# Kernel optimization log

Measured on AMD Instinct MI355X. Metric: run time of the kernel, lower is better.

The kernel has to match this reference:

```python
import jax, jax.numpy as jnp
import numpy as np

N = 100_000      # nodes
E = 1_600_000    # edges (avg degree 16)
IN = 128
H = 128
OUT = 2
G = 512          # graphs in the batch


def setup_inputs() -> dict:
    key = jax.random.key(0)
    ks = jax.random.split(key, 10)
    x = jax.random.normal(ks[0], (N, IN), dtype=jnp.float32)
    edge_index = jax.random.randint(ks[1], (2, E), 0, N, dtype=jnp.int64)
    edge_weight = jax.random.uniform(ks[2], (E,), dtype=jnp.float32)
    batch = jnp.sort(jax.random.randint(ks[3], (N,), 0, G, dtype=jnp.int64))
    s_in = 1.0 / np.sqrt(IN)
    s_h = 1.0 / np.sqrt(H)
    W1 = jax.random.normal(ks[4], (IN, H), dtype=jnp.float32) * s_in
    b1 = jnp.zeros((H,), dtype=jnp.float32)
    W2 = jax.random.normal(ks[5], (H, H), dtype=jnp.float32) * s_h
    b2 = jnp.zeros((H,), dtype=jnp.float32)
    Wl = jax.random.normal(ks[6], (H, OUT), dtype=jnp.float32) * s_h
    bl = jnp.zeros((OUT,), dtype=jnp.float32)
    return {"x": x, "edge_index": edge_index, "edge_weight": edge_weight,
            "batch": batch, "W1": W1, "b1": b1, "W2": W2, "b2": b2,
            "Wl": Wl, "bl": bl}


def _gcn_layer(x, W, b, row, col, ew, n):
    # PyG GCNConv: linear transform, symmetric-normalized scatter-add, bias.
    xw = x @ W                                           # [n, H]
    deg = jax.ops.segment_sum(ew, col, num_segments=n)    # weighted in-degree
    dis = jnp.where(deg > 0, jax.lax.rsqrt(deg), 0.0)
    norm = dis[row] * ew * dis[col]                       # [E+n]
    msg = xw[row] * norm[:, None]                         # gather + scale
    out = jax.ops.segment_sum(msg, col, num_segments=n)   # scatter-add to targets
    return out + b


def reference(x, edge_index, edge_weight, batch, W1, b1, W2, b2, Wl, bl):
    n = x.shape[0]
    # GCNConv default: add self-loops with weight 1.0 (gcn_norm fill_value=1)
    loop = jnp.arange(n, dtype=edge_index.dtype)
    row = jnp.concatenate([edge_index[0], loop])
    col = jnp.concatenate([edge_index[1], loop])
    ew = jnp.concatenate([edge_weight, jnp.ones((n,), edge_weight.dtype)])

    h = jax.nn.relu(_gcn_layer(x, W1, b1, row, col, ew, n))
    h = jax.nn.relu(_gcn_layer(h, W2, b2, row, col, ew, n))

    # global_mean_pool over batch ids
    cnt = jax.ops.segment_sum(jnp.ones((n,), h.dtype), batch, num_segments=G)
    pooled = jax.ops.segment_sum(h, batch, num_segments=G)
    pooled = pooled / jnp.maximum(cnt, 1.0)[:, None]      # [G, H]

    return pooled @ Wl + bl                               # [G, OUT]
```

## Files before the change

### kernel.cpp

```cpp
#include <hip/hip_runtime.h>
#include <hip/hip_fp16.h>


#define HDIM 128
typedef unsigned int uint;
typedef unsigned long long u64;
typedef _Float16 half8 __attribute__((ext_vector_type(8)));
typedef float f32x4 __attribute__((ext_vector_type(4)));
typedef float f32x2 __attribute__((ext_vector_type(2)));

#define NBUCK 391
#define BSTRIDE 8192
#define SCAT_BLOCKS 392
#define CHUNK 4096
#define QITER 16

template <typename AT>
__device__ __forceinline__ void gemm_body(
    const AT* __restrict__ A, const float* __restrict__ W,
    unsigned char* __restrict__ Y, int n, int nstrip, int tid, int bid,
    int nblk, char* smem) {
  char* Wt = smem;
  for (int t = tid; t < 2048; t += 256) {
    int c = t & 127;
    int k8 = t >> 7;
    const float* wp = W + (size_t)(k8 * 8) * HDIM + c;
    half8 hv;
#pragma unroll
    for (int m = 0; m < 8; ++m) hv[m] = (_Float16)wp[m * HDIM];
    int byte = c * 256 + k8 * 16;
    byte ^= ((c & 7) << 4);
    *(half8*)&Wt[byte] = hv;
  }
  __syncthreads();

  int wave = tid >> 6, lane = tid & 63;
  int l15 = lane & 15, l4 = lane >> 4;
  char* ep = smem + 32768 + wave * 2048;
  int stride = nblk * 4;
  for (int s = bid * 4 + wave; s < nstrip; s += stride) {
    int row0 = s << 4;
    int xrl = min(row0 + l15, n - 1);
    half8 bf[4];
    if constexpr (sizeof(AT) == 4) {
      const float* ap = (const float*)A + (size_t)xrl * HDIM + l4 * 8;
#pragma unroll
      for (int kk = 0; kk < 4; ++kk) {
        float4 u = *(const float4*)(ap + kk * 32);
        float4 v = *(const float4*)(ap + kk * 32 + 4);
        half8 h;
        h[0] = (_Float16)u.x; h[1] = (_Float16)u.y;
        h[2] = (_Float16)u.z; h[3] = (_Float16)u.w;
        h[4] = (_Float16)v.x; h[5] = (_Float16)v.y;
        h[6] = (_Float16)v.z; h[7] = (_Float16)v.w;
        bf[kk] = h;
      }
    } else {
      const half8* ap = (const half8*)((const _Float16*)A + (size_t)xrl * HDIM + l4 * 8);
#pragma unroll
      for (int kk = 0; kk < 4; ++kk) bf[kk] = ap[kk * 4];
    }
    f32x4 acc[8];
#pragma unroll
    for (int cf = 0; cf < 8; ++cf) acc[cf] = (f32x4){0.f, 0.f, 0.f, 0.f};
#pragma unroll
    for (int kk = 0; kk < 4; ++kk) {
#pragma unroll
      for (int cf = 0; cf < 8; ++cf) {
        int c = cf * 16 + l15;
        int byte = c * 256 + kk * 64 + l4 * 16;
        byte ^= ((c & 7) << 4);
        half8 af = *(half8*)&Wt[byte];
        acc[cf] = __builtin_amdgcn_mfma_f32_16x16x32_f16(af, bf[kk], acc[cf], 0, 0, 0);
      }
    }
#pragma unroll
    for (int cf = 0; cf < 8; ++cf) {
      int w = 0;
      w = __builtin_amdgcn_cvt_pk_fp8_f32(acc[cf][0], acc[cf][1], w, false);
      w = __builtin_amdgcn_cvt_pk_fp8_f32(acc[cf][2], acc[cf][3], w, true);
      int byte = l15 * 128 + ((cf * 16) ^ ((l15 & 7) << 4)) + l4 * 4;
      *(int*)&ep[byte] = w;
    }
    asm volatile("s_waitcnt lgkmcnt(0)" ::: "memory");
#pragma unroll
    for (int p = 0; p < 2; ++p) {
      int rl = p * 8 + (lane >> 3);
      int c16 = (lane & 7) * 16;
      int byte = rl * 128 + (c16 ^ ((rl & 7) << 4));
      uint4 v = *(uint4*)&ep[byte];
      int orow = row0 + rl;
      if (orow < n)
        *(uint4*)(Y + (size_t)orow * 128 + c16) = v;
    }
    asm volatile("s_waitcnt lgkmcnt(0)" ::: "memory");
  }
}

__global__ __launch_bounds__(256) void init_gstart_kernel(
    uint* __restrict__ gcur, const int* __restrict__ batch,
    int* __restrict__ start, int n, int G) {
  int bid = blockIdx.x, tid = threadIdx.x;
  if (bid < 2) {
    int t = bid * 256 + tid;
    if (t < NBUCK) gcur[t] = (uint)(t * BSTRIDE);
    return;
  }
  int i = (bid - 2) * 256 + tid;
  if (i >= n) return;
  int b = batch[i];
  if (i == 0) {
    for (int h = 0; h <= b; ++h) start[h] = 0;
  } else {
    int bp = batch[i - 1];
    for (int h = bp + 1; h <= b; ++h) start[h] = i;
  }
  if (i == n - 1) {
    for (int h = b + 1; h <= G; ++h) start[h] = n;
  }
}

__global__ __launch_bounds__(256) void scatter_gemm1_kernel(
    const int* __restrict__ row, const int* __restrict__ col,
    const float* __restrict__ ew, uint* __restrict__ gcur,
    uint2* __restrict__ rec, int E,
    const float* __restrict__ A, const float* __restrict__ W,
    unsigned char* __restrict__ Y, int n, int nstrip, int GBLK) {
  __shared__ __align__(16) char smem[40960];
  int bid = blockIdx.x, tid = threadIdx.x;
  if (bid % 3 == 0) {
    int sidx = bid / 3;
    uint* cntL = (uint*)smem;
    uint* baseL = cntL + NBUCK;
    for (int t = tid; t < NBUCK; t += 256) cntL[t] = 0;
    __syncthreads();
    int e0 = sidx * CHUNK + tid;
    uint pk[QITER];
#pragma unroll
    for (int q = 0; q < QITER; ++q) {
      int e = e0 + q * 256;
      pk[q] = 0xFFFFFFFFu;
      if (e < E) {
        uint c = (uint)col[e];
        uint b = c >> 8;
        uint r = atomicAdd(&cntL[b], 1u);
        pk[q] = (b << 21) | ((c & 255u) << 13) | r;
      }
    }
    __syncthreads();
    for (int t = tid; t < NBUCK; t += 256) {
      uint c = cntL[t];
      baseL[t] = c ? atomicAdd(&gcur[t], c) : 0;
    }
    __syncthreads();
#pragma unroll
    for (int q = 0; q < QITER; ++q) {
      int e = e0 + q * 256;
      if (e < E) {
        uint b = pk[q] >> 21;
        uint clo = (pk[q] >> 13) & 255u;
        uint rk = pk[q] & 8191u;
        uint slot = baseL[b] + rk;
        rec[slot] = make_uint2(((uint)row[e] << 8) | clo,
                               __float_as_uint(ew[e]));
      }
    }
    return;
  }
  int gidx = bid - bid / 3 - 1;
  gemm_body<float>(A, W, Y, n, nstrip, tid, gidx, GBLK, smem);
}

__global__ __launch_bounds__(512) void scan_buckets_kernel(
    const uint* __restrict__ gcur, uint* __restrict__ cbase,
    int* __restrict__ off, int n, int E) {
  __shared__ uint tmp[512];
  int tid = threadIdx.x;
  uint v = (tid < NBUCK) ? (gcur[tid] - (uint)(tid * BSTRIDE)) : 0;
  tmp[tid] = v;
  __syncthreads();
  for (int d = 1; d < 512; d <<= 1) {
    uint t = (tid >= d) ? tmp[tid - d] : 0;
    __syncthreads();
    tmp[tid] += t;
    __syncthreads();
  }
  if (tid < NBUCK) cbase[tid] = tmp[tid] - v;
  if (tid == 0) off[n] = E;
}

__global__ __launch_bounds__(256) void bucket_stats_kernel(
    const uint2* __restrict__ rec, const uint* __restrict__ gcur,
    const uint* __restrict__ cbase, float* __restrict__ dis,
    int* __restrict__ off, int n) {
  __shared__ uint degL[256];
  __shared__ uint cntL[256];
  __shared__ uint scn[256];
  int b = blockIdx.x, tid = threadIdx.x;
  degL[tid] = 0;
  cntL[tid] = 0;
  __syncthreads();
  uint s = (uint)(b * BSTRIDE);
  uint e = gcur[b];
  for (uint i = s + tid; i < e; i += 256) {
    uint2 r = rec[i];
    uint cl = r.x & 255u;
    atomicAdd(&cntL[cl], 1u);
    atomicAdd(&degL[cl], __float2uint_rn(__uint_as_float(r.y) * 65536.0f));
  }
  __syncthreads();
  uint v = cntL[tid];
  scn[tid] = v;
  __syncthreads();
  for (int d = 1; d < 256; d <<= 1) {
    uint t = (tid >= d) ? scn[tid - d] : 0;
    __syncthreads();
    scn[tid] += t;
    __syncthreads();
  }
  int c = b * 256 + tid;
  if (c < n) {
    off[c] = (int)(cbase[b] + scn[tid] - v);
    float deg = (float)degL[tid] * (1.0f / 65536.0f);
    dis[c] = rsqrtf(deg + 1.0f);
  }
}

__global__ __launch_bounds__(256) void csr_fill_kernel(
    const uint2* __restrict__ rec, const uint* __restrict__ gcur,
    const float* __restrict__ dis, const int* __restrict__ off,
    uint* __restrict__ csr, int n) {
  __shared__ uint baseL[256];
  __shared__ uint curL[256];
  int b = blockIdx.x, tid = threadIdx.x;
  int c = b * 256 + tid;
  baseL[tid] = (c < n) ? (uint)off[c] : 0;
  curL[tid] = 0;
  __syncthreads();
  uint s = (uint)(b * BSTRIDE);
  uint e = gcur[b];
  for (uint i = s + tid; i < e; i += 256) {
    uint2 rcd = rec[i];
    uint cl = rcd.x & 255u;
    uint r = rcd.x >> 8;
    uint slot = baseL[cl] + atomicAdd(&curL[cl], 1u);
    float ewv = __uint_as_float(rcd.y);
    uint nq = __float2uint_rn(dis[r] * ewv * 32768.0f);
    nq = min(nq, 32767u);
    csr[slot] = (r << 15) | nq;
  }
}

__global__ __launch_bounds__(256) void gemm_mfma_kernel(
    const _Float16* __restrict__ A, const float* __restrict__ W,
    unsigned char* __restrict__ Y, int n, int nstrip) {
  __shared__ __align__(16) char smem[40960];
  gemm_body<_Float16>(A, W, Y, n, nstrip, threadIdx.x, blockIdx.x, gridDim.x, smem);
}

__global__ __launch_bounds__(256) void agg_kernel(
    const uint* __restrict__ xw, const uint* __restrict__ csr,
    const float* __restrict__ dis, const int* __restrict__ off,
    const float* __restrict__ bias, uint* __restrict__ out, int n) {
  int node = blockIdx.x * 4 + (threadIdx.x >> 6);
  if (node >= n) return;
  int lane = threadIdx.x & 63;
  int hl = lane & 31;
  int par = lane >> 5;
  float dc = dis[node];
  float a0, a1, a2, a3;
  {
    uint v = xw[(size_t)node * 32 + hl];
    f32x2 lo = __builtin_amdgcn_cvt_pk_f32_fp8((int)v, false);
    f32x2 hi = __builtin_amdgcn_cvt_pk_f32_fp8((int)v, true);
    float sd = (par == 0) ? dc : 0.0f;
    a0 = sd * lo[0]; a1 = sd * lo[1]; a2 = sd * hi[0]; a3 = sd * hi[1];
  }
  const float qs = 1.0f / 32768.0f;
  int s = off[node], t = off[node + 1];
  int i = s;
  for (; i + 16 <= t; i += 16) {
    uint ee[8];
#pragma unroll
    for (int j = 0; j < 8; ++j) ee[j] = csr[i + 2 * j + par];
    uint vv[8];
#pragma unroll
    for (int j = 0; j < 8; ++j) vv[j] = xw[(size_t)(ee[j] >> 15) * 32 + hl];
#pragma unroll
    for (int j = 0; j < 8; ++j) {
      float nn = (float)(ee[j] & 0x7FFFu) * qs;
      f32x2 lo = __builtin_amdgcn_cvt_pk_f32_fp8((int)vv[j], false);
      f32x2 hi = __builtin_amdgcn_cvt_pk_f32_fp8((int)vv[j], true);
      a0 += nn * lo[0]; a1 += nn * lo[1]; a2 += nn * hi[0]; a3 += nn * hi[1];
    }
  }
  for (; i + 8 <= t; i += 8) {
    uint ee[4];
#pragma unroll
    for (int j = 0; j < 4; ++j) ee[j] = csr[i + 2 * j + par];
    uint vv[4];
#pragma unroll
    for (int j = 0; j < 4; ++j) vv[j] = xw[(size_t)(ee[j] >> 15) * 32 + hl];
#pragma unroll
    for (int j = 0; j < 4; ++j) {
      float nn = (float)(ee[j] & 0x7FFFu) * qs;
      f32x2 lo = __builtin_amdgcn_cvt_pk_f32_fp8((int)vv[j], false);
      f32x2 hi = __builtin_amdgcn_cvt_pk_f32_fp8((int)vv[j], true);
      a0 += nn * lo[0]; a1 += nn * lo[1]; a2 += nn * hi[0]; a3 += nn * hi[1];
    }
  }
  for (; i < t; i += 2) {
    if (i + par < t) {
      uint e = csr[i + par];
      uint v = xw[(size_t)(e >> 15) * 32 + hl];
      float nn = (float)(e & 0x7FFFu) * qs;
      f32x2 lo = __builtin_amdgcn_cvt_pk_f32_fp8((int)v, false);
      f32x2 hi = __builtin_amdgcn_cvt_pk_f32_fp8((int)v, true);
      a0 += nn * lo[0]; a1 += nn * lo[1]; a2 += nn * hi[0]; a3 += nn * hi[1];
    }
  }
  a0 += __shfl_xor(a0, 32);
  a1 += __shfl_xor(a1, 32);
  a2 += __shfl_xor(a2, 32);
  a3 += __shfl_xor(a3, 32);
  if (par == 0) {
    float4 b = *(const float4*)(bias + hl * 4);
    a0 = fmaxf(dc * a0 + b.x, 0.0f);
    a1 = fmaxf(dc * a1 + b.y, 0.0f);
    a2 = fmaxf(dc * a2 + b.z, 0.0f);
    a3 = fmaxf(dc * a3 + b.w, 0.0f);
    __half2 p0 = __floats2half2_rn(a0, a1);
    __half2 p1 = __floats2half2_rn(a2, a3);
    ((uint2*)out)[(size_t)node * 32 + hl] = make_uint2(*(uint*)&p0, *(uint*)&p1);
  }
}

__global__ __launch_bounds__(256) void pool_final_kernel(
    const uint* __restrict__ h, const int* __restrict__ start,
    const float* __restrict__ Wl, const float* __restrict__ bl,
    float* __restrict__ out) {
  __shared__ float2 red[256];
  int g = blockIdx.x;
  int grp = threadIdx.x >> 6, f = threadIdx.x & 63;
  int s = start[g], e = start[g + 1];
  float s0 = 0.0f, s1 = 0.0f;
  for (int r = s + grp; r < e; r += 4) {
    uint v = h[((size_t)r << 6) + f];
    float2 fv = __half22float2(*(const __half2*)&v);
    s0 += fv.x;
    s1 += fv.y;
  }
  red[threadIdx.x] = make_float2(s0, s1);
  __syncthreads();
  if (grp == 0) {
    float2 a = red[f], b = red[64 + f], c = red[128 + f], d = red[192 + f];
    float inv = 1.0f / (float)max(e - s, 1);
    float pv0 = (a.x + b.x + c.x + d.x) * inv;
    float pv1 = (a.y + b.y + c.y + d.y) * inv;
#pragma unroll
    for (int o = 0; o < 2; ++o) {
      float sdot = pv0 * Wl[4 * f + o] + pv1 * Wl[4 * f + 2 + o];
      for (int d2 = 32; d2 > 0; d2 >>= 1) sdot += __shfl_down(sdot, d2);
      if (f == 0) out[g * 2 + o] = sdot + bl[o];
    }
  }
}

extern "C" void kernel_launch(void* const* d_in, const int* in_sizes, int n_in,
                              void* d_out, int out_size, void* d_ws, size_t ws_size,
                              hipStream_t stream) {
  const float* x     = (const float*)d_in[0];
  const int*   ei    = (const int*)d_in[1];
  const float* ew    = (const float*)d_in[2];
  const int*   batch = (const int*)d_in[3];
  const float* W1    = (const float*)d_in[4];
  const float* b1    = (const float*)d_in[5];
  const float* W2    = (const float*)d_in[6];
  const float* b2    = (const float*)d_in[7];
  const float* Wl    = (const float*)d_in[8];
  const float* bl    = (const float*)d_in[9];
  float* out = (float*)d_out;

  const int N = in_sizes[0] / HDIM;
  const int E = in_sizes[2];
  const int G = out_size / 2;

  const int* row = ei;
  const int* col = ei + E;

  auto al = [](size_t v) { return (v + 255) & ~(size_t)255; };
  char* ws = (char*)d_ws;
  size_t o_gcur   = 0;
  size_t o_cbase  = o_gcur   + al(NBUCK * 4);
  size_t o_start  = o_cbase  + al(NBUCK * 4);
  size_t o_off    = o_start  + al(((size_t)G + 1) * 4);
  size_t o_dis    = o_off    + al(((size_t)N + 1) * 4);
  size_t o_rec    = o_dis    + al((size_t)N * 4);
  size_t o_csr    = o_rec    + al((size_t)NBUCK * BSTRIDE * 8);
  size_t o_xw     = o_csr    + al((size_t)E * 4);
  size_t o_h      = o_xw     + al((size_t)N * 128);

  uint*  gcur    = (uint*) (ws + o_gcur);
  uint*  cbase   = (uint*) (ws + o_cbase);
  int*   start   = (int*)  (ws + o_start);
  int*   off     = (int*)  (ws + o_off);
  float* dis     = (float*)(ws + o_dis);
  uint2* rec     = (uint2*)(ws + o_rec);
  uint*  csr     = (uint*) (ws + o_csr);
  unsigned char* xw = (unsigned char*)(ws + o_xw);
  uint*  hbuf    = (uint*) (ws + o_h);

  int NBg = (N + 255) / 256;
  int nstrip = (N + 15) / 16;
  int MB  = 1024;
  int AB  = (N + 3) / 4;
  int TOTAL_C = SCAT_BLOCKS * 3;
  int GBLK = TOTAL_C - SCAT_BLOCKS;

  init_gstart_kernel<<<2 + NBg, 256, 0, stream>>>(gcur, batch, start, N, G);

  scatter_gemm1_kernel<<<TOTAL_C, 256, 0, stream>>>(
      row, col, ew, gcur, rec, E, x, W1, xw, N, nstrip, GBLK);

  scan_buckets_kernel<<<1, 512, 0, stream>>>(gcur, cbase, off, N, E);

  bucket_stats_kernel<<<NBUCK, 256, 0, stream>>>(rec, gcur, cbase, dis, off, N);

  csr_fill_kernel<<<NBUCK, 256, 0, stream>>>(rec, gcur, dis, off, csr, N);

  agg_kernel<<<AB, 256, 0, stream>>>((const uint*)xw, csr, dis, off, b1, hbuf, N);

  gemm_mfma_kernel<<<MB, 256, 0, stream>>>((const _Float16*)hbuf, W2, xw, N, nstrip);
  agg_kernel<<<AB, 256, 0, stream>>>((const uint*)xw, csr, dis, off, b2, hbuf, N);

  pool_final_kernel<<<G, 256, 0, stream>>>(hbuf, start, Wl, bl, out);
}
```

Baseline: 201.6 us.

## Fold source normalization into xw rows, merge stats/fill, coalesce bucket scatter

Scatter blocks now stage their records in shared memory sorted by bucket and write them out contiguously, so global writes coalesce instead of landing at random slots. The bucket-stats and CSR-fill kernels are merged into one kernel. That kernel also pre-scales the layer-1 xw rows by the source node's dis, so the CSR weight no longer needs a random dis[row] gather. The layer-2 GEMM applies the same dis scaling in its epilogue. This saves a launch and scattered reads, at the cost of an extra read-modify-write pass over xw and fp8 re-quantisation after scaling, which may lose accuracy.

```diff
diff --git a/kernel.cpp b/kernel.cpp
--- a/kernel.cpp
+++ b/kernel.cpp
@@ -15,11 +15,11 @@
 #define CHUNK 4096
 #define QITER 16
 
-template <typename AT>
+template <typename AT, bool SCALE>
 __device__ __forceinline__ void gemm_body(
     const AT* __restrict__ A, const float* __restrict__ W,
-    unsigned char* __restrict__ Y, int n, int nstrip, int tid, int bid,
-    int nblk, char* smem) {
+    unsigned char* __restrict__ Y, const float* __restrict__ dsc,
+    int n, int nstrip, int tid, int bid, int nblk, char* smem) {
   char* Wt = smem;
   for (int t = tid; t < 2048; t += 256) {
     int c = t & 127;
@@ -74,11 +74,13 @@
         acc[cf] = __builtin_amdgcn_mfma_f32_16x16x32_f16(af, bf[kk], acc[cf], 0, 0, 0);
       }
     }
+    float ds = 1.0f;
+    if constexpr (SCALE) ds = dsc[xrl];
 #pragma unroll
     for (int cf = 0; cf < 8; ++cf) {
       int w = 0;
-      w = __builtin_amdgcn_cvt_pk_fp8_f32(acc[cf][0], acc[cf][1], w, false);
-      w = __builtin_amdgcn_cvt_pk_fp8_f32(acc[cf][2], acc[cf][3], w, true);
+      w = __builtin_amdgcn_cvt_pk_fp8_f32(acc[cf][0] * ds, acc[cf][1] * ds, w, false);
+      w = __builtin_amdgcn_cvt_pk_fp8_f32(acc[cf][2] * ds, acc[cf][3] * ds, w, true);
       int byte = l15 * 128 + ((cf * 16) ^ ((l15 & 7) << 4)) + l4 * 4;
       *(int*)&ep[byte] = w;
     }
@@ -130,8 +132,11 @@
   int bid = blockIdx.x, tid = threadIdx.x;
   if (bid % 3 == 0) {
     int sidx = bid / 3;
-    uint* cntL = (uint*)smem;
-    uint* baseL = cntL + NBUCK;
+    uint* cntL  = (uint*)smem;
+    uint* sbase = (uint*)(smem + 1568);
+    uint* gdel  = (uint*)(smem + 3136);
+    uint2* recL = (uint2*)(smem + 4736);
+    uint* tmp   = (uint*)(smem + 4736);
     for (int t = tid; t < NBUCK; t += 256) cntL[t] = 0;
     __syncthreads();
     int e0 = sidx * CHUNK + tid;
@@ -148,9 +153,28 @@
       }
     }
     __syncthreads();
+    uint v0 = (tid < NBUCK) ? cntL[tid] : 0;
+    uint v1 = (tid + 256 < NBUCK) ? cntL[tid + 256] : 0;
+    tmp[tid] = v0;
+    tmp[tid + 256] = v1;
+    __syncthreads();
+    for (int d = 1; d < 512; d <<= 1) {
+      uint a0 = (tid >= d) ? tmp[tid - d] : 0;
+      uint a1 = (tid + 256 >= d) ? tmp[tid + 256 - d] : 0;
+      __syncthreads();
+      tmp[tid] += a0;
+      tmp[tid + 256] += a1;
+      __syncthreads();
+    }
+    if (tid < NBUCK) sbase[tid] = tmp[tid] - v0;
+    if (tid + 256 < NBUCK) sbase[tid + 256] = tmp[tid + 256] - v1;
+    if (tid == NBUCK - 1 - 256) sbase[NBUCK] = tmp[NBUCK - 1];
+    __syncthreads();
+    uint tcount = sbase[NBUCK];
     for (int t = tid; t < NBUCK; t += 256) {
       uint c = cntL[t];
-      baseL[t] = c ? atomicAdd(&gcur[t], c) : 0;
+      uint gb = c ? atomicAdd(&gcur[t], c) : 0;
+      gdel[t] = gb - sbase[t];
     }
     __syncthreads();
 #pragma unroll
@@ -160,15 +184,27 @@
         uint b = pk[q] >> 21;
         uint clo = (pk[q] >> 13) & 255u;
         uint rk = pk[q] & 8191u;
-        uint slot = baseL[b] + rk;
-        rec[slot] = make_uint2(((uint)row[e] << 8) | clo,
-                               __float_as_uint(ew[e]));
+        recL[sbase[b] + rk] = make_uint2(((uint)row[e] << 8) | clo,
+                                         __float_as_uint(ew[e]));
       }
     }
+    __syncthreads();
+#pragma unroll
+    for (int q = 0; q < QITER; ++q) {
+      uint p = (uint)(q * 256 + tid);
+      if (p < tcount) {
+        int lo = 0, hi = NBUCK;
+        while (hi - lo > 1) {
+          int mid = (lo + hi) >> 1;
+          if (p >= sbase[mid]) lo = mid; else hi = mid;
+        }
+        rec[p + gdel[lo]] = recL[p];
+      }
+    }
     return;
   }
   int gidx = bid - bid / 3 - 1;
-  gemm_body<float>(A, W, Y, n, nstrip, tid, gidx, GBLK, smem);
+  gemm_body<float, false>(A, W, Y, nullptr, n, nstrip, tid, gidx, GBLK, smem);
 }
 
 __global__ __launch_bounds__(512) void scan_buckets_kernel(
@@ -189,13 +225,16 @@
   if (tid == 0) off[n] = E;
 }
 
-__global__ __launch_bounds__(256) void bucket_stats_kernel(
+__global__ __launch_bounds__(256) void stats_fill_kernel(
     const uint2* __restrict__ rec, const uint* __restrict__ gcur,
     const uint* __restrict__ cbase, float* __restrict__ dis,
-    int* __restrict__ off, int n) {
+    int* __restrict__ off, uint* __restrict__ xw, uint* __restrict__ csr,
+    int n) {
   __shared__ uint degL[256];
   __shared__ uint cntL[256];
   __shared__ uint scn[256];
+  __shared__ uint baseL[256];
+  __shared__ float disL[256];
   int b = blockIdx.x, tid = threadIdx.x;
   degL[tid] = 0;
   cntL[tid] = 0;
@@ -219,33 +258,41 @@
     __syncthreads();
   }
   int c = b * 256 + tid;
+  uint nodeBase = cbase[b] + scn[tid] - v;
+  float dcv = 0.0f;
   if (c < n) {
-    off[c] = (int)(cbase[b] + scn[tid] - v);
+    off[c] = (int)nodeBase;
     float deg = (float)degL[tid] * (1.0f / 65536.0f);
-    dis[c] = rsqrtf(deg + 1.0f);
-  }
-}
-
-__global__ __launch_bounds__(256) void csr_fill_kernel(
-    const uint2* __restrict__ rec, const uint* __restrict__ gcur,
-    const float* __restrict__ dis, const int* __restrict__ off,
-    uint* __restrict__ csr, int n) {
-  __shared__ uint baseL[256];
-  __shared__ uint curL[256];
-  int b = blockIdx.x, tid = threadIdx.x;
-  int c = b * 256 + tid;
-  baseL[tid] = (c < n) ? (uint)off[c] : 0;
-  curL[tid] = 0;
-  __syncthreads();
-  uint s = (uint)(b * BSTRIDE);
-  uint e = gcur[b];
+    dcv = rsqrtf(deg + 1.0f);
+    dis[c] = dcv;
+  }
+  baseL[tid] = nodeBase;
+  disL[tid] = dcv;
+  cntL[tid] = 0;
+  __syncthreads();
+  int node0 = b * 256;
+  int nloc = min(256, n - node0);
+  for (int j = 0; j < 32 && (tid >> 5) + 8 * j < nloc; ++j) {
+    int ln = (tid >> 5) + 8 * j;
+    int w = tid & 31;
+    float dl = disL[ln];
+    size_t idx = (size_t)(node0 + ln) * 32 + w;
+    uint val = xw[idx];
+    f32x2 lo = __builtin_amdgcn_cvt_pk_f32_fp8((int)val, false);
+    f32x2 hi = __builtin_amdgcn_cvt_pk_f32_fp8((int)val, true);
+    int o = 0;
+    o = __builtin_amdgcn_cvt_pk_fp8_f32(lo[0] * dl, lo[1] * dl, o, false);
+    o = __builtin_amdgcn_cvt_pk_fp8_f32(hi[0] * dl, hi[1] * dl, o, true);
+    xw[idx] = (uint)o;
+  }
+  __syncthreads();
   for (uint i = s + tid; i < e; i += 256) {
     uint2 rcd = rec[i];
     uint cl = rcd.x & 255u;
     uint r = rcd.x >> 8;
-    uint slot = baseL[cl] + atomicAdd(&curL[cl], 1u);
+    uint slot = baseL[cl] + atomicAdd(&cntL[cl], 1u);
     float ewv = __uint_as_float(rcd.y);
-    uint nq = __float2uint_rn(dis[r] * ewv * 32768.0f);
+    uint nq = __float2uint_rn(ewv * 32768.0f);
     nq = min(nq, 32767u);
     csr[slot] = (r << 15) | nq;
   }
@@ -253,9 +300,11 @@
 
 __global__ __launch_bounds__(256) void gemm_mfma_kernel(
     const _Float16* __restrict__ A, const float* __restrict__ W,
-    unsigned char* __restrict__ Y, int n, int nstrip) {
+    unsigned char* __restrict__ Y, const float* __restrict__ dis,
+    int n, int nstrip) {
   __shared__ __align__(16) char smem[40960];
-  gemm_body<_Float16>(A, W, Y, n, nstrip, threadIdx.x, blockIdx.x, gridDim.x, smem);
+  gemm_body<_Float16, true>(A, W, Y, dis, n, nstrip, threadIdx.x, blockIdx.x,
+                            gridDim.x, smem);
 }
 
 __global__ __launch_bounds__(256) void agg_kernel(
@@ -273,7 +322,7 @@
     uint v = xw[(size_t)node * 32 + hl];
     f32x2 lo = __builtin_amdgcn_cvt_pk_f32_fp8((int)v, false);
     f32x2 hi = __builtin_amdgcn_cvt_pk_f32_fp8((int)v, true);
-    float sd = (par == 0) ? dc : 0.0f;
+    float sd = (par == 0) ? 1.0f : 0.0f;
     a0 = sd * lo[0]; a1 = sd * lo[1]; a2 = sd * hi[0]; a3 = sd * hi[1];
   }
   const float qs = 1.0f / 32768.0f;
@@ -424,13 +473,13 @@
 
   scan_buckets_kernel<<<1, 512, 0, stream>>>(gcur, cbase, off, N, E);
 
-  bucket_stats_kernel<<<NBUCK, 256, 0, stream>>>(rec, gcur, cbase, dis, off, N);
-
-  csr_fill_kernel<<<NBUCK, 256, 0, stream>>>(rec, gcur, dis, off, csr, N);
+  stats_fill_kernel<<<NBUCK, 256, 0, stream>>>(rec, gcur, cbase, dis, off,
+                                               (uint*)xw, csr, N);
 
   agg_kernel<<<AB, 256, 0, stream>>>((const uint*)xw, csr, dis, off, b1, hbuf, N);
 
-  gemm_mfma_kernel<<<MB, 256, 0, stream>>>((const _Float16*)hbuf, W2, xw, N, nstrip);
+  gemm_mfma_kernel<<<MB, 256, 0, stream>>>((const _Float16*)hbuf, W2, xw, dis,
+                                           N, nstrip);
   agg_kernel<<<AB, 256, 0, stream>>>((const uint*)xw, csr, dis, off, b2, hbuf, N);
 
   pool_final_kernel<<<G, 256, 0, stream>>>(hbuf, start, Wl, bl, out);
```

Result: slower. 211.7 us (+5.0%).

## Split fp32-to-fp16 conversion into scatter kernel, fold bucket scan into stats

Applied to the files above, without the earlier changes.

The first GEMM is no longer fused with the edge scatter. Instead the scatter kernel's spare blocks convert x to an fp16 buffer, and a separate fp16 GEMM launch runs afterwards. The batch-start computation moves into the same scatter launch. The single-block bucket scan kernel is removed, and every bucket_stats block now redoes the 391-entry prefix scan itself. This trades an extra 25.6MB fp16 write and read, plus redundant scans, for fewer launches and a cheaper GEMM inner load.

```diff
diff --git a/kernel.cpp b/kernel.cpp
--- a/kernel.cpp
+++ b/kernel.cpp
@@ -15,9 +15,8 @@
 #define CHUNK 4096
 #define QITER 16
 
-template <typename AT>
-__device__ __forceinline__ void gemm_body(
-    const AT* __restrict__ A, const float* __restrict__ W,
+__device__ __forceinline__ void gemm_body16(
+    const _Float16* __restrict__ A, const float* __restrict__ W,
     unsigned char* __restrict__ Y, int n, int nstrip, int tid, int bid,
     int nblk, char* smem) {
   char* Wt = smem;
@@ -42,24 +41,9 @@
     int row0 = s << 4;
     int xrl = min(row0 + l15, n - 1);
     half8 bf[4];
-    if constexpr (sizeof(AT) == 4) {
-      const float* ap = (const float*)A + (size_t)xrl * HDIM + l4 * 8;
-#pragma unroll
-      for (int kk = 0; kk < 4; ++kk) {
-        float4 u = *(const float4*)(ap + kk * 32);
-        float4 v = *(const float4*)(ap + kk * 32 + 4);
-        half8 h;
-        h[0] = (_Float16)u.x; h[1] = (_Float16)u.y;
-        h[2] = (_Float16)u.z; h[3] = (_Float16)u.w;
-        h[4] = (_Float16)v.x; h[5] = (_Float16)v.y;
-        h[6] = (_Float16)v.z; h[7] = (_Float16)v.w;
-        bf[kk] = h;
-      }
-    } else {
-      const half8* ap = (const half8*)((const _Float16*)A + (size_t)xrl * HDIM + l4 * 8);
-#pragma unroll
-      for (int kk = 0; kk < 4; ++kk) bf[kk] = ap[kk * 4];
-    }
+    const half8* ap = (const half8*)(A + (size_t)xrl * HDIM + l4 * 8);
+#pragma unroll
+    for (int kk = 0; kk < 4; ++kk) bf[kk] = ap[kk * 4];
     f32x4 acc[8];
 #pragma unroll
     for (int cf = 0; cf < 8; ++cf) acc[cf] = (f32x4){0.f, 0.f, 0.f, 0.f};
@@ -97,41 +81,40 @@
   }
 }
 
-__global__ __launch_bounds__(256) void init_gstart_kernel(
-    uint* __restrict__ gcur, const int* __restrict__ batch,
-    int* __restrict__ start, int n, int G) {
-  int bid = blockIdx.x, tid = threadIdx.x;
-  if (bid < 2) {
-    int t = bid * 256 + tid;
-    if (t < NBUCK) gcur[t] = (uint)(t * BSTRIDE);
-    return;
-  }
-  int i = (bid - 2) * 256 + tid;
-  if (i >= n) return;
-  int b = batch[i];
-  if (i == 0) {
-    for (int h = 0; h <= b; ++h) start[h] = 0;
-  } else {
-    int bp = batch[i - 1];
-    for (int h = bp + 1; h <= b; ++h) start[h] = i;
-  }
-  if (i == n - 1) {
-    for (int h = b + 1; h <= G; ++h) start[h] = n;
-  }
-}
-
-__global__ __launch_bounds__(256) void scatter_gemm1_kernel(
+__global__ __launch_bounds__(256) void conv_scatter_kernel(
+    const float* __restrict__ x, _Float16* __restrict__ x16, int total_elems,
     const int* __restrict__ row, const int* __restrict__ col,
     const float* __restrict__ ew, uint* __restrict__ gcur,
     uint2* __restrict__ rec, int E,
-    const float* __restrict__ A, const float* __restrict__ W,
-    unsigned char* __restrict__ Y, int n, int nstrip, int GBLK) {
-  __shared__ __align__(16) char smem[40960];
+    const int* __restrict__ batch, int* __restrict__ start, int n, int G) {
+  __shared__ uint cntL[NBUCK];
+  __shared__ uint baseL[NBUCK];
   int bid = blockIdx.x, tid = threadIdx.x;
-  if (bid % 3 == 0) {
-    int sidx = bid / 3;
-    uint* cntL = (uint*)smem;
-    uint* baseL = cntL + NBUCK;
+  if (bid < 2) {
+  }
+  if (bid < 784 && (bid & 1) == 0) {
+    int sidx = bid >> 1;
+    if (sidx < NBUCK) {
+      size_t base = (size_t)sidx * 32768;
+#pragma unroll 4
+      for (int q = 0; q < 16; ++q) {
+        size_t i = base + (size_t)q * 2048 + (size_t)tid * 8;
+        if (i < (size_t)total_elems) {
+          float4 u = *(const float4*)(x + i);
+          float4 v = *(const float4*)(x + i + 4);
+          half8 h;
+          h[0] = (_Float16)u.x; h[1] = (_Float16)u.y;
+          h[2] = (_Float16)u.z; h[3] = (_Float16)u.w;
+          h[4] = (_Float16)v.x; h[5] = (_Float16)v.y;
+          h[6] = (_Float16)v.z; h[7] = (_Float16)v.w;
+          *(half8*)(x16 + i) = h;
+        }
+      }
+    }
+    return;
+  }
+  if (bid < 784) {
+    int sidx = bid >> 1;
     for (int t = tid; t < NBUCK; t += 256) cntL[t] = 0;
     __syncthreads();
     int e0 = sidx * CHUNK + tid;
@@ -160,46 +143,56 @@
         uint b = pk[q] >> 21;
         uint clo = (pk[q] >> 13) & 255u;
         uint rk = pk[q] & 8191u;
-        uint slot = baseL[b] + rk;
-        rec[slot] = make_uint2(((uint)row[e] << 8) | clo,
-                               __float_as_uint(ew[e]));
+        rec[baseL[b] + rk] = make_uint2(((uint)row[e] << 8) | clo,
+                                        __float_as_uint(ew[e]));
       }
     }
     return;
   }
-  int gidx = bid - bid / 3 - 1;
-  gemm_body<float>(A, W, Y, n, nstrip, tid, gidx, GBLK, smem);
-}
-
-__global__ __launch_bounds__(512) void scan_buckets_kernel(
-    const uint* __restrict__ gcur, uint* __restrict__ cbase,
-    int* __restrict__ off, int n, int E) {
-  __shared__ uint tmp[512];
-  int tid = threadIdx.x;
-  uint v = (tid < NBUCK) ? (gcur[tid] - (uint)(tid * BSTRIDE)) : 0;
-  tmp[tid] = v;
-  __syncthreads();
-  for (int d = 1; d < 512; d <<= 1) {
-    uint t = (tid >= d) ? tmp[tid - d] : 0;
-    __syncthreads();
-    tmp[tid] += t;
-    __syncthreads();
-  }
-  if (tid < NBUCK) cbase[tid] = tmp[tid] - v;
-  if (tid == 0) off[n] = E;
+  int i = (bid - 784) * 256 + tid;
+  if (i >= n) return;
+  int b = batch[i];
+  if (i == 0) {
+    for (int h = 0; h <= b; ++h) start[h] = 0;
+  } else {
+    int bp = batch[i - 1];
+    for (int h = bp + 1; h <= b; ++h) start[h] = i;
+  }
+  if (i == n - 1) {
+    for (int h = b + 1; h <= G; ++h) start[h] = n;
+  }
+}
+
+__global__ __launch_bounds__(256) void init_kernel(uint* __restrict__ gcur) {
+  int t = blockIdx.x * 256 + threadIdx.x;
+  if (t < NBUCK) gcur[t] = (uint)(t * BSTRIDE);
 }
 
 __global__ __launch_bounds__(256) void bucket_stats_kernel(
     const uint2* __restrict__ rec, const uint* __restrict__ gcur,
-    const uint* __restrict__ cbase, float* __restrict__ dis,
-    int* __restrict__ off, int n) {
+    float* __restrict__ dis, int* __restrict__ off, int n, int E) {
   __shared__ uint degL[256];
   __shared__ uint cntL[256];
   __shared__ uint scn[256];
+  __shared__ uint tmp[512];
   int b = blockIdx.x, tid = threadIdx.x;
   degL[tid] = 0;
   cntL[tid] = 0;
-  __syncthreads();
+  uint c0 = (tid < NBUCK) ? (gcur[tid] - (uint)(tid * BSTRIDE)) : 0;
+  uint c1 = (tid + 256 < NBUCK) ? (gcur[tid + 256] - (uint)((tid + 256) * BSTRIDE)) : 0;
+  tmp[tid] = c0;
+  tmp[tid + 256] = c1;
+  __syncthreads();
+  for (int d = 1; d < 512; d <<= 1) {
+    uint a0 = (tid >= d) ? tmp[tid - d] : 0;
+    uint a1 = (tid + 256 >= d) ? tmp[tid + 256 - d] : 0;
+    __syncthreads();
+    tmp[tid] += a0;
+    tmp[tid + 256] += a1;
+    __syncthreads();
+  }
+  uint cbase = tmp[b] - (gcur[b] - (uint)(b * BSTRIDE));
+  if (b == 0 && tid == 0) off[n] = E;
   uint s = (uint)(b * BSTRIDE);
   uint e = gcur[b];
   for (uint i = s + tid; i < e; i += 256) {
@@ -220,7 +213,7 @@
   }
   int c = b * 256 + tid;
   if (c < n) {
-    off[c] = (int)(cbase[b] + scn[tid] - v);
+    off[c] = (int)(cbase + scn[tid] - v);
     float deg = (float)degL[tid] * (1.0f / 65536.0f);
     dis[c] = rsqrtf(deg + 1.0f);
   }
@@ -255,7 +248,7 @@
     const _Float16* __restrict__ A, const float* __restrict__ W,
     unsigned char* __restrict__ Y, int n, int nstrip) {
   __shared__ __align__(16) char smem[40960];
-  gemm_body<_Float16>(A, W, Y, n, nstrip, threadIdx.x, blockIdx.x, gridDim.x, smem);
+  gemm_body16(A, W, Y, n, nstrip, threadIdx.x, blockIdx.x, gridDim.x, smem);
 }
 
 __global__ __launch_bounds__(256) void agg_kernel(
@@ -391,20 +384,20 @@
   auto al = [](size_t v) { return (v + 255) & ~(size_t)255; };
   char* ws = (char*)d_ws;
   size_t o_gcur   = 0;
-  size_t o_cbase  = o_gcur   + al(NBUCK * 4);
-  size_t o_start  = o_cbase  + al(NBUCK * 4);
+  size_t o_start  = o_gcur   + al(NBUCK * 4);
   size_t o_off    = o_start  + al(((size_t)G + 1) * 4);
   size_t o_dis    = o_off    + al(((size_t)N + 1) * 4);
-  size_t o_rec    = o_dis    + al((size_t)N * 4);
+  size_t o_x16    = o_dis    + al((size_t)N * 4);
+  size_t o_rec    = o_x16    + al((size_t)N * HDIM * 2);
   size_t o_csr    = o_rec    + al((size_t)NBUCK * BSTRIDE * 8);
   size_t o_xw     = o_csr    + al((size_t)E * 4);
   size_t o_h      = o_xw     + al((size_t)N * 128);
 
   uint*  gcur    = (uint*) (ws + o_gcur);
-  uint*  cbase   = (uint*) (ws + o_cbase);
   int*   start   = (int*)  (ws + o_start);
   int*   off     = (int*)  (ws + o_off);
   float* dis     = (float*)(ws + o_dis);
+  _Float16* x16  = (_Float16*)(ws + o_x16);
   uint2* rec     = (uint2*)(ws + o_rec);
   uint*  csr     = (uint*) (ws + o_csr);
   unsigned char* xw = (unsigned char*)(ws + o_xw);
@@ -414,17 +407,15 @@
   int nstrip = (N + 15) / 16;
   int MB  = 1024;
   int AB  = (N + 3) / 4;
-  int TOTAL_C = SCAT_BLOCKS * 3;
-  int GBLK = TOTAL_C - SCAT_BLOCKS;
-
-  init_gstart_kernel<<<2 + NBg, 256, 0, stream>>>(gcur, batch, start, N, G);
-
-  scatter_gemm1_kernel<<<TOTAL_C, 256, 0, stream>>>(
-      row, col, ew, gcur, rec, E, x, W1, xw, N, nstrip, GBLK);
-
-  scan_buckets_kernel<<<1, 512, 0, stream>>>(gcur, cbase, off, N, E);
-
-  bucket_stats_kernel<<<NBUCK, 256, 0, stream>>>(rec, gcur, cbase, dis, off, N);
+
+  init_kernel<<<2, 256, 0, stream>>>(gcur);
+
+  conv_scatter_kernel<<<784 + NBg, 256, 0, stream>>>(
+      x, x16, N * HDIM, row, col, ew, gcur, rec, E, batch, start, N, G);
+
+  gemm_mfma_kernel<<<MB, 256, 0, stream>>>(x16, W1, xw, N, nstrip);
+
+  bucket_stats_kernel<<<NBUCK, 256, 0, stream>>>(rec, gcur, dis, off, N, E);
 
   csr_fill_kernel<<<NBUCK, 256, 0, stream>>>(rec, gcur, dis, off, csr, N);
 
```

After: 213.5 us. +5.9%, slower.
